# Optimization experiments

Hardware: AMD Instinct MI355X
Metric: run time of the kernel (lower is better)

## Reference

```python
import jax, jax.numpy as jnp
import numpy as np
from jax import lax

# Mamba2 config (matches init_kwargs + mamba_ssm defaults)
B_SZ, SEQ = 8, 2048
D_MODEL, D_STATE, EXPAND, HEADDIM = 1024, 128, 2, 64
D_INNER = EXPAND * D_MODEL            # 2048
NHEADS = D_INNER // HEADDIM           # 32
NGROUPS, D_CONV, CHUNK = 1, 4, 128
CONV_DIM = D_INNER + 2 * NGROUPS * D_STATE
D_IN_PROJ = 2 * D_INNER + 2 * NGROUPS * D_STATE + NHEADS
VAR_NUM, EPS = 3, 1e-5


def setup_inputs() -> dict:
    key = jax.random.key(0)
    ks = jax.random.split(key, 10)
    return {
        "embed_data": jax.random.normal(ks[0], (B_SZ, SEQ, D_MODEL), jnp.float32),
        "in_proj_w": jax.random.normal(ks[1], (D_IN_PROJ, D_MODEL), jnp.float32) * 0.02,
        "conv_w": jax.random.normal(ks[2], (CONV_DIM, D_CONV), jnp.float32) * 0.2,
        "conv_b": jnp.zeros((CONV_DIM,), jnp.float32),
        "dt_bias": jnp.log(jnp.expm1(jax.random.uniform(ks[3], (NHEADS,), jnp.float32, 1e-3, 0.1))),
        "A_log": jnp.log(jax.random.uniform(ks[4], (NHEADS,), jnp.float32, 1.0, 16.0)),
        "D": jnp.ones((NHEADS,), jnp.float32),
        "norm_w": jnp.ones((D_INNER,), jnp.float32),
        "out_proj_w": jax.random.normal(ks[5], (D_MODEL, D_INNER), jnp.float32) * 0.02,
        "dec_w": jax.random.normal(ks[6], (VAR_NUM, D_MODEL), jnp.float32) * 0.02,
        "dec_b": jnp.zeros((VAR_NUM,), jnp.float32),
    }


def _segsum(a):
    # a: (b,h,c,L) -> (b,h,c,L,L) lower-triangular segment sums
    L = a.shape[-1]
    cs = jnp.cumsum(a, -1)
    ss = cs[..., :, None] - cs[..., None, :]
    mask = jnp.tril(jnp.ones((L, L), bool))
    return jnp.where(mask, ss, -jnp.inf)


def _ssd(x, dt, A, Bm, Cm):
    # x:(b,l,h,p) dt:(b,l,h) A:(h,) Bm,Cm:(b,l,n); chunked SSD scan (Mamba2)
    b, l, h, p = x.shape
    n = Bm.shape[-1]
    c = l // CHUNK
    xc = x.reshape(b, c, CHUNK, h, p)
    dtc = dt.reshape(b, c, CHUNK, h)
    Bc = Bm.reshape(b, c, CHUNK, n)
    Cc = Cm.reshape(b, c, CHUNK, n)
    ac = (dt * A).reshape(b, c, CHUNK, h).transpose(0, 3, 1, 2)  # (b,h,c,L)
    acs = jnp.cumsum(ac, -1)
    Lmat = jnp.exp(_segsum(ac))                                   # (b,h,c,L,L)
    xdt = xc * dtc[..., None]
    # intra-chunk (diagonal block) outputs
    CB = jnp.einsum('bcln,bcsn->bcls', Cc, Bc)
    Y_diag = jnp.einsum('bcls,bhcls,bcshp->bclhp', CB, Lmat, xdt)
    # per-chunk final states
    decay_states = jnp.exp(acs[..., -1:] - acs)                   # (b,h,c,L)
    states = jnp.einsum('bcln,bhcl,bclhp->bchpn', Bc, decay_states, xdt)
    chunk_decay = jnp.exp(acs[..., -1])                           # (b,h,c)
    def step(carry, inp):
        st, dec = inp
        return carry * dec[..., None, None] + st, carry
    _, states_in = lax.scan(step, jnp.zeros((b, h, p, n), x.dtype),
                            (jnp.moveaxis(states, 1, 0), jnp.moveaxis(chunk_decay, 2, 0)))
    states_in = jnp.moveaxis(states_in, 0, 1)                     # (b,c,h,p,n)
    # inter-chunk (off-diagonal) contribution
    Y_off = jnp.einsum('bcln,bchpn,bhcl->bclhp', Cc, states_in, jnp.exp(acs))
    return (Y_diag + Y_off).reshape(b, l, h, p)


def reference(embed_data, in_proj_w, conv_w, conv_b, dt_bias, A_log, D, norm_w, out_proj_w, dec_w, dec_b):
    b, l, _ = embed_data.shape
    zxbcdt = embed_data @ in_proj_w.T                             # (b,l,D_IN_PROJ)
    z = zxbcdt[..., :D_INNER]
    xBC = zxbcdt[..., D_INNER:D_INNER + CONV_DIM]
    dt = jax.nn.softplus(zxbcdt[..., D_INNER + CONV_DIM:] + dt_bias)  # (b,l,h)
    # causal depthwise conv1d + SiLU
    xt = lax.conv_general_dilated(xBC.transpose(0, 2, 1), conv_w[:, None, :], (1,),
                                  [(D_CONV - 1, 0)], feature_group_count=CONV_DIM,
                                  dimension_numbers=('NCH', 'OIH', 'NCH'))
    xBC = jax.nn.silu(xt.transpose(0, 2, 1) + conv_b)
    x = xBC[..., :D_INNER].reshape(b, l, NHEADS, HEADDIM)
    Bm = xBC[..., D_INNER:D_INNER + D_STATE]
    Cm = xBC[..., D_INNER + D_STATE:]
    A = -jnp.exp(A_log)
    y = _ssd(x, dt, A, Bm, Cm) + D[None, None, :, None] * x
    # gated RMSNorm
    y = y.reshape(b, l, D_INNER) * jax.nn.silu(z)
    y = y * lax.rsqrt(jnp.mean(y * y, -1, keepdims=True) + EPS) * norm_w
    hidden = y @ out_proj_w.T
    pred = hidden @ dec_w.T + dec_b
    return pred, hidden
```

## Files before the change

### kernel.cpp

```cpp
#include <hip/hip_runtime.h>
#include <cstdint>

#define DEVI __device__ __forceinline__

typedef unsigned short u16;
typedef unsigned int u32;
typedef __attribute__((ext_vector_type(4))) float f32x4;
typedef __attribute__((ext_vector_type(8))) u16 u16x8;
typedef __attribute__((ext_vector_type(4))) u16 u16x4;
typedef __attribute__((ext_vector_type(8))) __bf16 bf16x8;

#define SEQL 2048
#define NBATCH 8
#define MROWS (NBATCH*SEQL)
#define DMODEL 1024
#define DINNER 2048
#define NHEADS 32
#define HEADD 64
#define DSTATE 128
#define CONVD 2304
#define NPROJ 4384
#define NPROJP 4608
#define CHUNKL 128
#define NCHUNK 16
#define PADC 136

DEVI float bf2f(u16 v){ u32 u = ((u32)v)<<16; return __builtin_bit_cast(float,u); }
DEVI u16 f2bf(float f){ u32 u = __builtin_bit_cast(u32,f); u32 r = (u + 0x7fffu + ((u>>16)&1u))>>16; return (u16)r; }

DEVI void gld_lds16(const void* g, void* lds){
  __builtin_amdgcn_global_load_lds(
    (const __attribute__((address_space(1))) void*)(uintptr_t)g,
    (__attribute__((address_space(3))) void*)(u32)(uintptr_t)lds, 16, 0, 0);
}

DEVI f32x4 MFMA(u16x8 a, u16x8 b, f32x4 c){
  return __builtin_amdgcn_mfma_f32_16x16x32_bf16(
      __builtin_bit_cast(bf16x8,a), __builtin_bit_cast(bf16x8,b), c, 0,0,0);
}

__global__ void k_sentinel(float* o){ o[0] = 12345.0f; }

__global__ __launch_bounds__(256) void k_cvt3(const float* __restrict__ e, u16* __restrict__ eb,
    const float* __restrict__ w1, u16* __restrict__ w1b,
    const float* __restrict__ w2, u16* __restrict__ w2b)
{
  int bid = blockIdx.x;
  const float* src; u16* dst; long n; long base;
  if (bid < 16384){ src = e;  dst = eb;  n = (long)MROWS*DMODEL;  base = (long)bid*1024; }
  else if (bid < 20992){ src = w1; dst = w1b; n = (long)NPROJ*DMODEL; base = (long)(bid-16384)*1024; }
  else { src = w2; dst = w2b; n = (long)DMODEL*DINNER; base = (long)(bid-20992)*1024; }
  long idx = base + (long)threadIdx.x*4;
  u16x4 o;
  if (idx < n){
    f32x4 v = *(const f32x4*)(src+idx);
    o[0]=f2bf(v[0]); o[1]=f2bf(v[1]); o[2]=f2bf(v[2]); o[3]=f2bf(v[3]);
  } else { o[0]=0; o[1]=0; o[2]=0; o[3]=0; }
  *(u16x4*)(dst+idx) = o;
}

#define STG(mat, h, ts) do { \
    const int d_ = (ts) & 1; \
    const size_t ko_ = (size_t)(((ts) < NT) ? (ts) : (NT-1)) * 64; \
    gld_lds16(sbase[mat][h][0] + ko_, (char*)lds + (mat)*65536 + (d_*2+(h))*16384 + tid*16); \
    gld_lds16(sbase[mat][h][1] + ko_, (char*)lds + (mat)*65536 + (d_*2+(h))*16384 + 8192 + tid*16); \
  } while(0)

#define LDA8(AF, d_, qm) { \
    _Pragma("unroll") for (int mf=0; mf<4; mf++) \
    _Pragma("unroll") for (int ks=0; ks<2; ks++) \
      AF[mf][ks] = *(const u16x8*)(lds + (size_t)((d_)*2+wm)*8192 + ((qm)*64+mf*16+lidx)*64 + ((ks*4+krow)^(lidx&7))*8); }

#define LDB4(BF, d_, qn) { \
    _Pragma("unroll") for (int nf=0; nf<2; nf++) \
    _Pragma("unroll") for (int ks=0; ks<2; ks++) \
      BF[nf][ks] = *(const u16x8*)(lds + 32768 + (size_t)((d_)*2+(wn>>1))*8192 + ((wn&1)*64+(qn)*32+nf*16+lidx)*64 + ((ks*4+krow)^(lidx&7))*8); }

#define MMAQ(QM, QN, AF, BF) { \
    _Pragma("unroll") for (int mf=0; mf<4; mf++) \
    _Pragma("unroll") for (int nf=0; nf<2; nf++) \
    _Pragma("unroll") for (int ks=0; ks<2; ks++) \
      acc[(QM)*4+mf][(QN)*2+nf] = MFMA(AF[mf][ks], BF[nf][ks], acc[(QM)*4+mf][(QN)*2+nf]); }

#define LHINT asm volatile("s_waitcnt lgkmcnt(8)" ::: "memory");

#define BAR1 __builtin_amdgcn_sched_barrier(0); __builtin_amdgcn_s_barrier(); \
    asm volatile("s_waitcnt lgkmcnt(0)" ::: "memory"); __builtin_amdgcn_sched_barrier(0); \
    __builtin_amdgcn_s_setprio(1);
#define BAR2 __builtin_amdgcn_s_setprio(0); __builtin_amdgcn_sched_barrier(0); \
    __builtin_amdgcn_s_barrier(); __builtin_amdgcn_sched_barrier(0);

template<int MODE>
__global__ __launch_bounds__(512, 2) void k_gemm8(const u16* __restrict__ A, const u16* __restrict__ Bt,
    const int K, const int Ndim, float* __restrict__ outF,
    u16* __restrict__ z_out, u16* __restrict__ xbc_out, float* __restrict__ dtraw_out)
{
  extern __shared__ u16 lds[];
  const int NT = K >> 6;
  const int tid = threadIdx.x;
  const int lane = tid & 63, wid = tid >> 6;
  const int wm = wid >> 2, wn = wid & 3;
  const int lidx = lane & 15, krow = lane >> 4;
  const int nmt = gridDim.x, nnt = gridDim.y;
  const int nwg = nmt * nnt;
  const int orig = blockIdx.y * nmt + blockIdx.x;
  const int qq = nwg >> 3, rr = nwg & 7;
  const int xcd = orig & 7, li = orig >> 3;
  const int pid = (xcd < rr ? xcd*(qq+1) : rr*(qq+1) + (xcd-rr)*qq) + li;
  const int GM = 8;
  const int npg = GM * nnt;
  const int gid = pid / npg;
  const int rem = pid % npg;
  const int m0 = (gid*GM + (rem & (GM-1))) * 256;
  const int n0 = (rem / GM) * 256;

  f32x4 acc[8][4];
  const f32x4 zf = {0.f,0.f,0.f,0.f};
  #pragma unroll
  for (int i=0;i<8;i++)
    #pragma unroll
    for (int j=0;j<4;j++) acc[i][j] = zf;

  const int r0 = tid >> 3;
  const int gsw = ((tid & 7) ^ (r0 & 7)) * 8;
  const u16* sbase[2][2][2];
  #pragma unroll
  for (int h=0; h<2; h++)
    #pragma unroll
    for (int L=0; L<2; L++){
      sbase[0][h][L] = A  + (size_t)(m0 + h*128 + L*64 + r0)*K + gsw;
      sbase[1][h][L] = Bt + (size_t)(n0 + h*128 + L*64 + r0)*K + gsw;
    }

  STG(0,0,0); STG(0,1,0); STG(1,0,0); STG(1,1,0);
  asm volatile("s_waitcnt vmcnt(4)" ::: "memory");
  STG(0,0,1); STG(0,1,1); STG(1,0,1);
  asm volatile("s_waitcnt vmcnt(6)" ::: "memory");
  __builtin_amdgcn_sched_barrier(0);
  __builtin_amdgcn_s_barrier();
  __builtin_amdgcn_sched_barrier(0);

  u16x8 af[4][2], bf0[2][2], bf1[2][2];
  for (int t = 0; t < NT; t += 2){
    LDA8(af, 0, 0); LDB4(bf0, 0, 0); STG(1,1,t+1); LHINT;
    BAR1; MMAQ(0,0,af,bf0); BAR2;
    LDB4(bf1, 0, 1);
    BAR1; MMAQ(0,1,af,bf1); BAR2;
    LDA8(af, 0, 1); STG(1,0,t+2);
    BAR1; MMAQ(1,1,af,bf1); BAR2;
    STG(0,0,t+2); STG(0,1,t+2);
    asm volatile("s_waitcnt vmcnt(6)" ::: "memory");
    BAR1; MMAQ(1,0,af,bf0); BAR2;
    LDA8(af, 1, 0); LDB4(bf0, 1, 0); STG(1,1,t+2); LHINT;
    BAR1; MMAQ(0,0,af,bf0); BAR2;
    LDB4(bf1, 1, 1);
    BAR1; MMAQ(0,1,af,bf1); BAR2;
    LDA8(af, 1, 1); STG(1,0,t+3);
    BAR1; MMAQ(1,1,af,bf1); BAR2;
    STG(0,0,t+3); STG(0,1,t+3);
    asm volatile("s_waitcnt vmcnt(6)" ::: "memory");
    BAR1; MMAQ(1,0,af,bf0); BAR2;
  }
  asm volatile("s_waitcnt vmcnt(0)" ::: "memory");

  #pragma unroll
  for (int im=0; im<8; im++)
    #pragma unroll
    for (int in=0; in<4; in++)
      #pragma unroll
      for (int r=0; r<4; r++){
        int gm = m0 + wm*128 + im*16 + krow*4 + r;
        int gn = n0 + wn*64 + in*16 + lidx;
        float v = acc[im][in][r];
        if (MODE==0){
          outF[(long)gm*Ndim + gn] = v;
        } else {
          if (gn < DINNER) z_out[(long)gm*DINNER + gn] = f2bf(v);
          else if (gn < DINNER+CONVD) xbc_out[(long)gm*CONVD + (gn-DINNER)] = f2bf(v);
          else if (gn < NPROJ) dtraw_out[(long)gm*NHEADS + (gn-DINNER-CONVD)] = v;
        }
      }
}

__global__ __launch_bounds__(128) void k_dtprep(const float* __restrict__ dtraw, const float* __restrict__ dt_bias,
    const float* __restrict__ A_log, float* __restrict__ dt_t, float* __restrict__ acs_t)
{
  int b = blockIdx.x >> 9;
  int h = (blockIdx.x >> 4) & 31;
  int c = blockIdx.x & 15;
  int l = threadIdx.x;
  int gl = c*128 + l;
  float raw = dtraw[((long)(b*SEQL + gl))*NHEADS + h] + dt_bias[h];
  float dt = (raw > 20.f) ? raw : log1pf(expf(raw));
  float A = -expf(A_log[h]);
  float ac = dt*A;
  __shared__ float ss[128];
  ss[l] = ac; __syncthreads();
  for (int o=1;o<128;o<<=1){
    float v = (l>=o)? ss[l-o] : 0.f;
    __syncthreads();
    ss[l] += v;
    __syncthreads();
  }
  float acs = ss[l];
  dt_t[((long)(b*NHEADS+h))*SEQL + gl] = dt;
  acs_t[((long)(b*NHEADS+h))*SEQL + gl] = acs;
}

__global__ __launch_bounds__(256) void k_conv(const u16* __restrict__ xbc, const float* __restrict__ conv_w,
    const float* __restrict__ conv_b, const float* __restrict__ dt_t,
    u16* __restrict__ xdtT, u16* __restrict__ BTt, u16* __restrict__ CTt)
{
  __shared__ u16 sm[131*64];
  int idx = blockIdx.x;
  int b = idx / 576; int rem = idx % 576; int cbk = rem >> 4; int lb = rem & 15;
  int ch0 = cbk*64, l0 = lb*128;
  for (int g = threadIdx.x; g < 131*8; g += 256){
    int r = g >> 3, cg = g & 7;
    int gl = l0 - 3 + r;
    u16x8 v;
    if (gl >= 0) v = *(const u16x8*)(xbc + ((long)(b*SEQL+gl))*CONVD + ch0 + cg*8);
    else { v[0]=0;v[1]=0;v[2]=0;v[3]=0;v[4]=0;v[5]=0;v[6]=0;v[7]=0; }
    *(u16x8*)(&sm[r*64 + cg*8]) = v;
  }
  __syncthreads();
  int ci = threadIdx.x & 63, g4 = threadIdx.x >> 6;
  int chg = ch0 + ci;
  f32x4 wv = *(const f32x4*)(conv_w + chg*4);
  float bia = conv_b[chg];
  bool isX = chg < DINNER;
  int h = chg >> 6; if (h > 31) h = 31;
  int p = chg & 63;
  const float* dtrow = dt_t + ((long)(b*NHEADS+h))*SEQL + l0 + g4*32;
  u16x8 ov[4];
  #pragma unroll
  for (int i=0;i<32;i++){
    int lr = g4*32 + i;
    float a = bia + wv[0]*bf2f(sm[(lr+0)*64+ci]) + wv[1]*bf2f(sm[(lr+1)*64+ci])
                  + wv[2]*bf2f(sm[(lr+2)*64+ci]) + wv[3]*bf2f(sm[(lr+3)*64+ci]);
    float s = a / (1.f + __expf(-a));
    if (isX) s *= dtrow[i];
    ov[i>>3][i&7] = f2bf(s);
  }
  u16* dst;
  if (isX)                      dst = xdtT + (((long)(b*NHEADS+h))*HEADD + p)*SEQL + l0 + g4*32;
  else if (chg < DINNER+DSTATE) dst = BTt + ((long)(b*DSTATE + (chg-DINNER)))*SEQL + l0 + g4*32;
  else                          dst = CTt + ((long)(b*DSTATE + (chg-DINNER-DSTATE)))*SEQL + l0 + g4*32;
  #pragma unroll
  for (int q=0;q<4;q++) *(u16x8*)(dst + q*8) = ov[q];
}

__global__ __launch_bounds__(256) void k_cbpar(const u16* __restrict__ BTt, const u16* __restrict__ CTt,
    const u16* __restrict__ xdtT, const float* __restrict__ acs_t,
    u16* __restrict__ CBm, u16* __restrict__ Cn, u16* __restrict__ states)
{
  __shared__ __align__(16) char smem[69632];
  const int tid = threadIdx.x;
  const int lane = tid & 63, wid = tid >> 6;
  const int lidx = lane & 15, krow = lane >> 4;
  const f32x4 zf = {0.f,0.f,0.f,0.f};
  if (blockIdx.x < 128){
    u16* Cl = (u16*)smem;
    u16* Bl = (u16*)(smem + 34816);
    int b = blockIdx.x >> 4, c = blockIdx.x & 15;
    for (int g = tid; g < 2048; g += 256){
      int n = g >> 4, lg = g & 15;
      u16x8 vc = *(const u16x8*)(CTt + ((long)(b*DSTATE+n))*SEQL + c*CHUNKL + lg*8);
      u16x8 vb = *(const u16x8*)(BTt + ((long)(b*DSTATE+n))*SEQL + c*CHUNKL + lg*8);
      #pragma unroll
      for (int j=0;j<8;j++){
        Cl[(lg*8+j)*136 + n] = vc[j];
        Bl[(lg*8+j)*136 + n] = vb[j];
      }
    }
    __syncthreads();
    const int wr = wid & 1, wc2 = wid >> 1;
    f32x4 acc[4][4];
    #pragma unroll
    for (int i=0;i<4;i++)
      #pragma unroll
      for (int j=0;j<4;j++) acc[i][j] = zf;
    #pragma unroll
    for (int k0=0;k0<128;k0+=32){
      u16x8 af[4], bfv[4];
      #pragma unroll
      for (int i=0;i<4;i++){
        af[i]  = *(const u16x8*)(&Cl[(wr*64+i*16+lidx)*136 + k0 + krow*8]);
        bfv[i] = *(const u16x8*)(&Bl[(wc2*64+i*16+lidx)*136 + k0 + krow*8]);
      }
      #pragma unroll
      for (int i=0;i<4;i++)
        #pragma unroll
        for (int j=0;j<4;j++)
          acc[i][j] = MFMA(af[i], bfv[j], acc[i][j]);
    }
    long base = ((long)(b*16+c))*128*128;
    #pragma unroll
    for (int i=0;i<4;i++)
      #pragma unroll
      for (int j=0;j<4;j++)
        #pragma unroll
        for (int r=0;r<4;r++){
          int l = wr*64+i*16+krow*4+r;
          int s = wc2*64+j*16+lidx;
          CBm[base + (long)l*128 + s] = f2bf(acc[i][j][r]);
        }
    for (int g = tid; g < 2048; g += 256){
      int l = g >> 4, ng = g & 15;
      u16x8 o;
      #pragma unroll
      for (int j=0;j<8;j++) o[j] = Cl[l*136 + ng*8 + j];
      *(u16x8*)(Cn + ((long)(b*SEQL + c*CHUNKL + l))*DSTATE + ng*8) = o;
    }
  } else {
    u16* Bs = (u16*)smem;
    u16* Xs = (u16*)(smem + 34816);
    float* acs_s = (float*)(smem + 52224);
    float* dec_s = (float*)(smem + 52736);
    const int idx = blockIdx.x - 128;
    const int c = idx & 15, bh = idx >> 4, b = bh >> 5;
    const int wps = wid & 1, wns = wid >> 1;
    const float* acs_g = acs_t + (long)bh*SEQL + c*128;
    const u16* X_g = xdtT + (long)bh*HEADD*SEQL + c*128;
    const u16* B_g = BTt + (long)b*DSTATE*SEQL + c*128;
    if (tid < 128) acs_s[tid] = acs_g[tid];
    __syncthreads();
    if (tid < 128) dec_s[tid] = __expf(acs_s[127] - acs_s[tid]);
    __syncthreads();
    for (int g = tid; g < 2048; g += 256){
      int n = g >> 4, lg = g & 15;
      u16x8 v = *(const u16x8*)(B_g + (long)n*SEQL + lg*8);
      u16x8 o;
      #pragma unroll
      for (int j=0;j<8;j++) o[j] = f2bf(bf2f(v[j])*dec_s[lg*8+j]);
      *(u16x8*)(&Bs[n*PADC + lg*8]) = o;
    }
    for (int g = tid; g < 1024; g += 256){
      int p = g >> 4, lg = g & 15;
      *(u16x8*)(&Xs[p*PADC + lg*8]) = *(const u16x8*)(X_g + (long)p*SEQL + lg*8);
    }
    __syncthreads();
    f32x4 accS[2][4];
    #pragma unroll
    for (int i=0;i<2;i++){ accS[i][0]=zf; accS[i][1]=zf; accS[i][2]=zf; accS[i][3]=zf; }
    #pragma unroll
    for (int k0=0;k0<128;k0+=32){
      u16x8 as2[2], bs2[4];
      #pragma unroll
      for (int i=0;i<2;i++) as2[i] = *(const u16x8*)(&Xs[(wps*32+i*16+lidx)*PADC + k0 + krow*8]);
      #pragma unroll
      for (int j=0;j<4;j++) bs2[j] = *(const u16x8*)(&Bs[(wns*64+j*16+lidx)*PADC + k0 + krow*8]);
      #pragma unroll
      for (int i=0;i<2;i++)
        #pragma unroll
        for (int j=0;j<4;j++)
          accS[i][j] = MFMA(as2[i], bs2[j], accS[i][j]);
    }
    u16* Sg = states + (long)idx*8192;
    #pragma unroll
    for (int i=0;i<2;i++)
      #pragma unroll
      for (int j=0;j<4;j++)
        #pragma unroll
        for (int r=0;r<4;r++){
          int p = wps*32 + i*16 + krow*4 + r;
          int n = wns*64 + j*16 + lidx;
          Sg[p*128 + n] = f2bf(accS[i][j][r]);
        }
  }
}

__global__ __launch_bounds__(256) void k_scan(u16* __restrict__ states, const float* __restrict__ acs_t)
{
  long gid = (long)blockIdx.x*256 + threadIdx.x;
  int bh = (int)(gid >> 11);
  int q = (int)(gid & 2047);
  __shared__ float cds[16];
  if (threadIdx.x < 16) cds[threadIdx.x] = __expf(acs_t[(long)bh*SEQL + threadIdx.x*128 + 127]);
  __syncthreads();
  u16* p = states + (long)bh*NCHUNK*8192 + q*4;
  u16x4 sv[16];
  #pragma unroll
  for (int c=0;c<16;c++) sv[c] = *(const u16x4*)(p + c*8192);
  float c0=0.f,c1=0.f,c2=0.f,c3=0.f;
  #pragma unroll
  for (int c=0;c<16;c++){
    u16x4 o; o[0]=f2bf(c0); o[1]=f2bf(c1); o[2]=f2bf(c2); o[3]=f2bf(c3);
    *(u16x4*)(p + c*8192) = o;
    float cd = cds[c];
    c0 = c0*cd + bf2f(sv[c][0]);
    c1 = c1*cd + bf2f(sv[c][1]);
    c2 = c2*cd + bf2f(sv[c][2]);
    c3 = c3*cd + bf2f(sv[c][3]);
  }
}

__global__ __launch_bounds__(256) void k_yoff(
    const u16* __restrict__ Cng, const u16* __restrict__ xdtT, const u16* __restrict__ CBm,
    const u16* __restrict__ SI, const float* __restrict__ acs_t, const float* __restrict__ dt_t,
    const float* __restrict__ Dparam, u16* __restrict__ y)
{
  __shared__ u16 Ts[128*PADC];
  __shared__ u16 Us[64*PADC];
  __shared__ float acs_s[128], dtr_s[128], eacs_s[128];
  const int idx = blockIdx.x;
  const int c = idx & 15, bh = idx >> 4, b = bh >> 5, h = bh & 31;
  const int tid = threadIdx.x, lane = tid & 63, wid = tid >> 6;
  const int lidx = lane & 15, krow = lane >> 4;
  const int wl = wid & 1, wp = wid >> 1;
  const float Dh = Dparam[h];
  const float* acs_g = acs_t + (long)bh*SEQL + c*128;
  const float* dt_g  = dt_t  + (long)bh*SEQL + c*128;
  const u16* X_g = xdtT + (long)bh*HEADD*SEQL + c*128;
  const u16* C_g = Cng + ((long)(b*SEQL + c*128))*DSTATE;
  const u16* CB_g = CBm + ((long)(b*NCHUNK + c))*CHUNKL*CHUNKL;
  const u16* SI_g = SI + (long)idx*8192;
  if (tid < 128){ acs_s[tid] = acs_g[tid]; dtr_s[tid] = dt_g[tid]; }
  __syncthreads();
  if (tid < 128) eacs_s[tid] = __expf(acs_s[tid]);
  __syncthreads();
  {
    int l = tid >> 1, s0 = (tid & 1)*64;
    float al = acs_s[l];
    #pragma unroll
    for (int qq=0;qq<8;qq++){
      u16x8 v = *(const u16x8*)(CB_g + (long)l*CHUNKL + s0 + qq*8);
      u16x8 o;
      #pragma unroll
      for (int j=0;j<8;j++){
        int s = s0 + qq*8 + j;
        float pv = (s <= l) ? bf2f(v[j]) * __expf(al - acs_s[s]) : 0.f;
        o[j] = f2bf(pv);
      }
      *(u16x8*)(&Ts[l*PADC + s0 + qq*8]) = o;
    }
  }
  for (int g = tid; g < 1024; g += 256){
    int p = g >> 4, lg = g & 15;
    *(u16x8*)(&Us[p*PADC + lg*8]) = *(const u16x8*)(X_g + (long)p*SEQL + lg*8);
  }
  __syncthreads();
  const f32x4 zf = {0.f,0.f,0.f,0.f};
  f32x4 accY[4][2];
  #pragma unroll
  for (int i=0;i<4;i++){ accY[i][0]=zf; accY[i][1]=zf; }
  #pragma unroll
  for (int k0=0;k0<128;k0+=32){
    u16x8 af[4], bfv[2];
    #pragma unroll
    for (int i=0;i<4;i++) af[i] = *(const u16x8*)(&Ts[(wl*64+i*16+lidx)*PADC + k0 + krow*8]);
    #pragma unroll
    for (int j=0;j<2;j++) bfv[j] = *(const u16x8*)(&Us[(wp*32+j*16+lidx)*PADC + k0 + krow*8]);
    #pragma unroll
    for (int i=0;i<4;i++)
      #pragma unroll
      for (int j=0;j<2;j++)
        accY[i][j] = MFMA(af[i], bfv[j], accY[i][j]);
  }
  #pragma unroll
  for (int i=0;i<4;i++)
    #pragma unroll
    for (int j=0;j<2;j++)
      #pragma unroll
      for (int r=0;r<4;r++){
        int l = wl*64 + i*16 + krow*4 + r;
        int p = wp*32 + j*16 + lidx;
        accY[i][j][r] += Dh * bf2f(Us[p*PADC + l]) / dtr_s[l];
      }
  __syncthreads();
  for (int g = tid; g < 2048; g += 256){
    int l = g >> 4, cb = g & 15;
    u16x8 v = *(const u16x8*)(C_g + (long)l*DSTATE + cb*8);
    float e = eacs_s[l];
    u16x8 o;
    #pragma unroll
    for (int j=0;j<8;j++) o[j] = f2bf(bf2f(v[j])*e);
    *(u16x8*)(&Ts[l*PADC + cb*8]) = o;
  }
  for (int g = tid; g < 1024; g += 256){
    int p = g >> 4, lg = g & 15;
    *(u16x8*)(&Us[p*PADC + lg*8]) = *(const u16x8*)(SI_g + p*128 + lg*8);
  }
  __syncthreads();
  #pragma unroll
  for (int k0=0;k0<128;k0+=32){
    u16x8 af[4], bfv[2];
    #pragma unroll
    for (int i=0;i<4;i++) af[i] = *(const u16x8*)(&Ts[(wl*64+i*16+lidx)*PADC + k0 + krow*8]);
    #pragma unroll
    for (int j=0;j<2;j++) bfv[j] = *(const u16x8*)(&Us[(wp*32+j*16+lidx)*PADC + k0 + krow*8]);
    #pragma unroll
    for (int i=0;i<4;i++)
      #pragma unroll
      for (int j=0;j<2;j++)
        accY[i][j] = MFMA(af[i], bfv[j], accY[i][j]);
  }
  #pragma unroll
  for (int i=0;i<4;i++)
    #pragma unroll
    for (int j=0;j<2;j++)
      #pragma unroll
      for (int r=0;r<4;r++){
        int l = wl*64 + i*16 + krow*4 + r;
        int p = wp*32 + j*16 + lidx;
        y[((long)(b*SEQL + c*128 + l))*DINNER + h*HEADD + p] = f2bf(accY[i][j][r]);
      }
}

__global__ __launch_bounds__(256) void k_ssd(
    const u16* __restrict__ Cng, const u16* __restrict__ BTt, const u16* __restrict__ xdtT,
    const u16* __restrict__ CBm, const float* __restrict__ acs_t, const float* __restrict__ dt_t,
    const float* __restrict__ Dparam, u16* __restrict__ y)
{
  __shared__ u16 Cs[128*PADC];
  __shared__ u16 Bs[128*PADC];
  __shared__ u16 Ps[128*PADC];
  __shared__ u16 Xs[64*PADC];
  __shared__ float carry[64*132];
  __shared__ float acs_s[128], eacs_s[128], dec_s[128], dtr_s[128];
  const int bh = blockIdx.x;
  const int b = bh >> 5, h = bh & 31;
  const int tid = threadIdx.x, lane = tid & 63, wid = tid >> 6;
  const int lidx = lane & 15, krow = lane >> 4;
  const int wl = wid & 1, wp = wid >> 1;
  const int wps = wid & 1, wns = wid >> 1;
  for (int i = tid; i < 64*132; i += 256) carry[i] = 0.f;
  const float Dh = Dparam[h];
  const float* acs_g = acs_t + (long)bh*SEQL;
  const float* dt_g = dt_t + (long)bh*SEQL;
  const u16* X_g = xdtT + (long)bh*HEADD*SEQL;
  const u16* B_g = BTt + (long)b*DSTATE*SEQL;
  const u16* C_g = Cng + (long)b*SEQL*DSTATE;
  const u16* CB_g = CBm + (long)b*NCHUNK*CHUNKL*CHUNKL;
  const f32x4 zf = {0.f,0.f,0.f,0.f};
  for (int c=0;c<NCHUNK;c++){
    __syncthreads();
    if (tid < 128){ acs_s[tid] = acs_g[c*128+tid]; dtr_s[tid] = dt_g[c*128+tid]; }
    __syncthreads();
    if (tid < 128){ float a = acs_s[tid]; eacs_s[tid] = __expf(a); dec_s[tid] = __expf(acs_s[127]-a); }
    __syncthreads();
    for (int g = tid; g < 2048; g += 256){
      int l = g >> 4, cb = g & 15;
      u16x8 v = *(const u16x8*)(C_g + ((long)(c*128+l))*DSTATE + cb*8);
      float e = eacs_s[l];
      u16x8 o;
      #pragma unroll
      for (int j=0;j<8;j++) o[j] = f2bf(bf2f(v[j])*e);
      *(u16x8*)(&Cs[l*PADC + cb*8]) = o;
    }
    for (int g = tid; g < 2048; g += 256){
      int n = g >> 4, lg = g & 15;
      u16x8 v = *(const u16x8*)(B_g + (long)n*SEQL + c*128 + lg*8);
      u16x8 o;
      #pragma unroll
      for (int j=0;j<8;j++) o[j] = f2bf(bf2f(v[j])*dec_s[lg*8+j]);
      *(u16x8*)(&Bs[n*PADC + lg*8]) = o;
    }
    for (int g = tid; g < 1024; g += 256){
      int p = g >> 4, lg = g & 15;
      *(u16x8*)(&Xs[p*PADC + lg*8]) = *(const u16x8*)(X_g + (long)p*SEQL + c*128 + lg*8);
    }
    {
      int l = tid >> 1, s0 = (tid & 1)*64;
      float al = acs_s[l];
      #pragma unroll
      for (int q=0;q<8;q++){
        u16x8 v = *(const u16x8*)(CB_g + ((long)(c*128+l))*CHUNKL + s0 + q*8);
        u16x8 o;
        #pragma unroll
        for (int j=0;j<8;j++){
          int s = s0 + q*8 + j;
          float pv = (s <= l) ? bf2f(v[j]) * __expf(al - acs_s[s]) : 0.f;
          o[j] = f2bf(pv);
        }
        *(u16x8*)(&Ps[l*PADC + s0 + q*8]) = o;
      }
    }
    __syncthreads();
    f32x4 accY[4][2];
    f32x4 accS[2][4];
    #pragma unroll
    for (int i=0;i<4;i++){ accY[i][0]=zf; accY[i][1]=zf; }
    #pragma unroll
    for (int i=0;i<2;i++){ accS[i][0]=zf; accS[i][1]=zf; accS[i][2]=zf; accS[i][3]=zf; }
    #pragma unroll
    for (int k0=0;k0<128;k0+=32){
      u16x8 af[4], bfv[2];
      #pragma unroll
      for (int i=0;i<4;i++) af[i] = *(const u16x8*)(&Cs[(wl*64+i*16+lidx)*PADC + k0 + krow*8]);
      #pragma unroll
      for (int j=0;j<2;j++){
        const float* cp = &carry[(wp*32+j*16+lidx)*132 + k0 + krow*8];
        f32x4 c0 = *(const f32x4*)cp;
        f32x4 c1 = *(const f32x4*)(cp+4);
        u16x8 o;
        o[0]=f2bf(c0[0]); o[1]=f2bf(c0[1]); o[2]=f2bf(c0[2]); o[3]=f2bf(c0[3]);
        o[4]=f2bf(c1[0]); o[5]=f2bf(c1[1]); o[6]=f2bf(c1[2]); o[7]=f2bf(c1[3]);
        bfv[j] = o;
      }
      #pragma unroll
      for (int i=0;i<4;i++)
        #pragma unroll
        for (int j=0;j<2;j++)
          accY[i][j] = MFMA(af[i], bfv[j], accY[i][j]);
    }
    #pragma unroll
    for (int k0=0;k0<128;k0+=32){
      u16x8 af[4], bfv[2];
      #pragma unroll
      for (int i=0;i<4;i++) af[i] = *(const u16x8*)(&Ps[(wl*64+i*16+lidx)*PADC + k0 + krow*8]);
      #pragma unroll
      for (int j=0;j<2;j++) bfv[j] = *(const u16x8*)(&Xs[(wp*32+j*16+lidx)*PADC + k0 + krow*8]);
      #pragma unroll
      for (int i=0;i<4;i++)
        #pragma unroll
        for (int j=0;j<2;j++)
          accY[i][j] = MFMA(af[i], bfv[j], accY[i][j]);
    }
    #pragma unroll
    for (int k0=0;k0<128;k0+=32){
      u16x8 as2[2], bs2[4];
      #pragma unroll
      for (int i=0;i<2;i++) as2[i] = *(const u16x8*)(&Xs[(wps*32+i*16+lidx)*PADC + k0 + krow*8]);
      #pragma unroll
      for (int j=0;j<4;j++) bs2[j] = *(const u16x8*)(&Bs[(wns*64+j*16+lidx)*PADC + k0 + krow*8]);
      #pragma unroll
      for (int i=0;i<2;i++)
        #pragma unroll
        for (int j=0;j<4;j++)
          accS[i][j] = MFMA(as2[i], bs2[j], accS[i][j]);
    }
    __syncthreads();
    float cd = __expf(acs_s[127]);
    #pragma unroll
    for (int i=0;i<2;i++)
      #pragma unroll
      for (int j=0;j<4;j++)
        #pragma unroll
        for (int r=0;r<4;r++){
          int p = wps*32 + i*16 + krow*4 + r;
          int n = wns*64 + j*16 + lidx;
          carry[p*132+n] = carry[p*132+n]*cd + accS[i][j][r];
        }
    #pragma unroll
    for (int i=0;i<4;i++)
      #pragma unroll
      for (int j=0;j<2;j++)
        #pragma unroll
        for (int r=0;r<4;r++){
          int l = wl*64 + i*16 + krow*4 + r;
          int p = wp*32 + j*16 + lidx;
          float xv = bf2f(Xs[p*PADC + l]) / dtr_s[l];
          float val = accY[i][j][r] + Dh*xv;
          y[((long)(b*SEQL + c*128 + l))*DINNER + h*HEADD + p] = f2bf(val);
        }
  }
}

__global__ __launch_bounds__(256) void k_gate(const u16* __restrict__ y, const u16* __restrict__ z,
    const float* __restrict__ norm_w, u16* __restrict__ out)
{
  long row = blockIdx.x;
  const u16* yr = y + row*DINNER;
  const u16* zr = z + row*DINNER;
  int t = threadIdx.x;
  u16x8 yy = *(const u16x8*)(yr + t*8);
  u16x8 zz = *(const u16x8*)(zr + t*8);
  float g[8]; float ss = 0.f;
  #pragma unroll
  for (int j=0;j<8;j++){
    float zfv = bf2f(zz[j]);
    float sg = zfv / (1.f + __expf(-zfv));
    float gv = bf2f(yy[j]) * sg;
    g[j] = gv; ss += gv*gv;
  }
  #pragma unroll
  for (int o=32;o>0;o>>=1) ss += __shfl_down(ss, o);
  __shared__ float part[4];
  int lane = t & 63, wid = t>>6;
  if (lane==0) part[wid] = ss;
  __syncthreads();
  float tot = part[0]+part[1]+part[2]+part[3];
  float inv = rsqrtf(tot*(1.f/DINNER) + 1e-5f);
  u16x8 o;
  #pragma unroll
  for (int j=0;j<8;j++) o[j] = f2bf(g[j]*inv*norm_w[t*8+j]);
  *(u16x8*)(out + row*DINNER + t*8) = o;
}

__global__ __launch_bounds__(256) void k_pred(const float* __restrict__ hid, const float* __restrict__ dec_w,
    const float* __restrict__ dec_b, float* __restrict__ pred)
{
  int t = threadIdx.x;
  long row = (long)blockIdx.x*8 + (t>>5);
  int lk = t & 31;
  const float* hr = hid + row*DMODEL;
  float a0=0.f,a1=0.f,a2=0.f;
  #pragma unroll
  for (int i=0;i<8;i++){
    f32x4 hv = *(const f32x4*)(hr + lk*4 + i*128);
    f32x4 w0 = *(const f32x4*)(dec_w + 0*DMODEL + lk*4 + i*128);
    f32x4 w1 = *(const f32x4*)(dec_w + 1*DMODEL + lk*4 + i*128);
    f32x4 w2 = *(const f32x4*)(dec_w + 2*DMODEL + lk*4 + i*128);
    a0 += hv[0]*w0[0]+hv[1]*w0[1]+hv[2]*w0[2]+hv[3]*w0[3];
    a1 += hv[0]*w1[0]+hv[1]*w1[1]+hv[2]*w1[2]+hv[3]*w1[3];
    a2 += hv[0]*w2[0]+hv[1]*w2[1]+hv[2]*w2[2]+hv[3]*w2[3];
  }
  #pragma unroll
  for (int o=16;o>0;o>>=1){
    a0 += __shfl_down(a0,o,32); a1 += __shfl_down(a1,o,32); a2 += __shfl_down(a2,o,32);
  }
  if (lk==0){
    pred[row*3+0] = a0 + dec_b[0];
    pred[row*3+1] = a1 + dec_b[1];
    pred[row*3+2] = a2 + dec_b[2];
  }
}

extern "C" void kernel_launch(void* const* d_in, const int* in_sizes, int n_in,
                              void* d_out, int out_size, void* d_ws, size_t ws_size,
                              hipStream_t stream)
{
  const float* embed      = (const float*)d_in[0];
  const float* in_proj_w  = (const float*)d_in[1];
  const float* conv_w     = (const float*)d_in[2];
  const float* conv_b     = (const float*)d_in[3];
  const float* dt_bias    = (const float*)d_in[4];
  const float* A_log      = (const float*)d_in[5];
  const float* Dp         = (const float*)d_in[6];
  const float* norm_w     = (const float*)d_in[7];
  const float* out_proj_w = (const float*)d_in[8];
  const float* dec_w      = (const float*)d_in[9];
  const float* dec_b      = (const float*)d_in[10];

  char* ws = (char*)d_ws;
  size_t off = 0;
  auto alloc = [&](size_t bytes)->void*{ void* p = ws + off; off += (bytes + 255) & ~(size_t)255; return p; };

  u16* xbc = (u16*)alloc((size_t)MROWS*CONVD*2);
  u16* yb  = xbc;
  u16* R2  = (u16*)alloc((size_t)MROWS*DINNER*2);
  u16* Ebf = R2;
  u16* W1  = R2 + (size_t)MROWS*DMODEL;
  u16* xdtT  = R2;
  u16* ynorm = R2;
  float* dtraw = (float*)alloc((size_t)MROWS*NHEADS*4);
  float* dt_t  = (float*)alloc((size_t)NBATCH*NHEADS*SEQL*4);
  float* acs   = (float*)alloc((size_t)NBATCH*NHEADS*SEQL*4);
  u16* BTt   = (u16*)alloc((size_t)NBATCH*DSTATE*SEQL*2);
  u16* CTt   = (u16*)alloc((size_t)NBATCH*DSTATE*SEQL*2);
  u16* Cn    = (u16*)alloc((size_t)NBATCH*SEQL*DSTATE*2);
  u16* CBm   = (u16*)alloc((size_t)NBATCH*NCHUNK*CHUNKL*CHUNKL*2);
  u16* W2    = (u16*)alloc((size_t)DMODEL*DINNER*2);

  size_t off_base = off;
  u16* S = (u16*)alloc((size_t)NBATCH*NHEADS*NCHUNK*HEADD*DSTATE*2);
  bool use_par = (off <= ws_size);

  if (off_base > ws_size){
    k_sentinel<<<1,1,0,stream>>>((float*)d_out);
    return;
  }

  float* pred   = (float*)d_out;
  float* hidden = (float*)d_out + (size_t)MROWS*3;
  u16* zb = (u16*)hidden;

  hipFuncSetAttribute((const void*)k_gemm8<1>, hipFuncAttributeMaxDynamicSharedMemorySize, 131072);
  hipFuncSetAttribute((const void*)k_gemm8<0>, hipFuncAttributeMaxDynamicSharedMemorySize, 131072);

  k_cvt3<<<23040,256,0,stream>>>(embed, Ebf, in_proj_w, W1, out_proj_w, W2);
  {
    dim3 g1(64, NPROJP/256);
    k_gemm8<1><<<g1,512,131072,stream>>>(Ebf, W1, DMODEL, 0, nullptr, zb, xbc, dtraw);
  }
  k_dtprep<<<4096,128,0,stream>>>(dtraw, dt_bias, A_log, dt_t, acs);
  k_conv<<<4608,256,0,stream>>>(xbc, conv_w, conv_b, dt_t, xdtT, BTt, CTt);
  k_cbpar<<<(use_par ? 4224 : 128),256,0,stream>>>(BTt, CTt, xdtT, acs, CBm, Cn, S);
  if (use_par){
    k_scan<<<2048,256,0,stream>>>(S, acs);
    k_yoff<<<4096,256,0,stream>>>(Cn, xdtT, CBm, S, acs, dt_t, Dp, yb);
  } else {
    k_ssd<<<256,256,0,stream>>>(Cn, BTt, xdtT, CBm, acs, dt_t, Dp, yb);
  }
  k_gate<<<16384,256,0,stream>>>(yb, zb, norm_w, ynorm);
  {
    dim3 g2(64, DMODEL/256);
    k_gemm8<0><<<g2,512,131072,stream>>>(ynorm, W2, DINNER, DMODEL, hidden, nullptr, nullptr, nullptr);
  }
  k_pred<<<2048,256,0,stream>>>(hidden, dec_w, dec_b, pred);
}
```

Baseline: 532.1 us.

## Drop LDS wait hint in GEMM, slide conv window, batch gate rows per block

Three unrelated tweaks. The GEMM main loop loses its partial lgkmcnt wait hint before the first barrier. The depthwise conv keeps a sliding window of four converted values in registers, so each step does one LDS load and conversion instead of four. The gate/RMSNorm kernel handles four rows per block with norm weights hoisted, cutting the grid by 4x at the cost of an extra barrier per row and less parallelism.

```diff
diff --git a/kernel.cpp b/kernel.cpp
--- a/kernel.cpp
+++ b/kernel.cpp
@@ -81,8 +81,6 @@
     _Pragma("unroll") for (int nf=0; nf<2; nf++) \
     _Pragma("unroll") for (int ks=0; ks<2; ks++) \
       acc[(QM)*4+mf][(QN)*2+nf] = MFMA(AF[mf][ks], BF[nf][ks], acc[(QM)*4+mf][(QN)*2+nf]); }
-
-#define LHINT asm volatile("s_waitcnt lgkmcnt(8)" ::: "memory");
 
 #define BAR1 __builtin_amdgcn_sched_barrier(0); __builtin_amdgcn_s_barrier(); \
     asm volatile("s_waitcnt lgkmcnt(0)" ::: "memory"); __builtin_amdgcn_sched_barrier(0); \
@@ -142,7 +140,7 @@
 
   u16x8 af[4][2], bf0[2][2], bf1[2][2];
   for (int t = 0; t < NT; t += 2){
-    LDA8(af, 0, 0); LDB4(bf0, 0, 0); STG(1,1,t+1); LHINT;
+    LDA8(af, 0, 0); LDB4(bf0, 0, 0); STG(1,1,t+1);
     BAR1; MMAQ(0,0,af,bf0); BAR2;
     LDB4(bf1, 0, 1);
     BAR1; MMAQ(0,1,af,bf1); BAR2;
@@ -151,7 +149,7 @@
     STG(0,0,t+2); STG(0,1,t+2);
     asm volatile("s_waitcnt vmcnt(6)" ::: "memory");
     BAR1; MMAQ(1,0,af,bf0); BAR2;
-    LDA8(af, 1, 0); LDB4(bf0, 1, 0); STG(1,1,t+2); LHINT;
+    LDA8(af, 1, 0); LDB4(bf0, 1, 0); STG(1,1,t+2);
     BAR1; MMAQ(0,0,af,bf0); BAR2;
     LDB4(bf1, 1, 1);
     BAR1; MMAQ(0,1,af,bf1); BAR2;
@@ -233,11 +231,15 @@
   int p = chg & 63;
   const float* dtrow = dt_t + ((long)(b*NHEADS+h))*SEQL + l0 + g4*32;
   u16x8 ov[4];
+  const int baseR = g4*32;
+  float w0, w1 = bf2f(sm[(baseR+0)*64+ci]);
+  float w2 = bf2f(sm[(baseR+1)*64+ci]);
+  float w3 = bf2f(sm[(baseR+2)*64+ci]);
   #pragma unroll
   for (int i=0;i<32;i++){
-    int lr = g4*32 + i;
-    float a = bia + wv[0]*bf2f(sm[(lr+0)*64+ci]) + wv[1]*bf2f(sm[(lr+1)*64+ci])
-                  + wv[2]*bf2f(sm[(lr+2)*64+ci]) + wv[3]*bf2f(sm[(lr+3)*64+ci]);
+    w0 = w1; w1 = w2; w2 = w3;
+    w3 = bf2f(sm[(baseR+i+3)*64+ci]);
+    float a = bia + wv[0]*w0 + wv[1]*w1 + wv[2]*w2 + wv[3]*w3;
     float s = a / (1.f + __expf(-a));
     if (isX) s *= dtrow[i];
     ov[i>>3][i&7] = f2bf(s);
@@ -660,32 +662,37 @@
 __global__ __launch_bounds__(256) void k_gate(const u16* __restrict__ y, const u16* __restrict__ z,
     const float* __restrict__ norm_w, u16* __restrict__ out)
 {
-  long row = blockIdx.x;
-  const u16* yr = y + row*DINNER;
-  const u16* zr = z + row*DINNER;
   int t = threadIdx.x;
-  u16x8 yy = *(const u16x8*)(yr + t*8);
-  u16x8 zz = *(const u16x8*)(zr + t*8);
-  float g[8]; float ss = 0.f;
-  #pragma unroll
-  for (int j=0;j<8;j++){
-    float zfv = bf2f(zz[j]);
-    float sg = zfv / (1.f + __expf(-zfv));
-    float gv = bf2f(yy[j]) * sg;
-    g[j] = gv; ss += gv*gv;
-  }
-  #pragma unroll
-  for (int o=32;o>0;o>>=1) ss += __shfl_down(ss, o);
+  int lane = t & 63, wid = t>>6;
   __shared__ float part[4];
-  int lane = t & 63, wid = t>>6;
-  if (lane==0) part[wid] = ss;
-  __syncthreads();
-  float tot = part[0]+part[1]+part[2]+part[3];
-  float inv = rsqrtf(tot*(1.f/DINNER) + 1e-5f);
-  u16x8 o;
-  #pragma unroll
-  for (int j=0;j<8;j++) o[j] = f2bf(g[j]*inv*norm_w[t*8+j]);
-  *(u16x8*)(out + row*DINNER + t*8) = o;
+  float nw[8];
+  #pragma unroll
+  for (int j=0;j<8;j++) nw[j] = norm_w[t*8+j];
+  #pragma unroll
+  for (int rr=0; rr<4; rr++){
+    long row = (long)blockIdx.x*4 + rr;
+    u16x8 yy = *(const u16x8*)(y + row*DINNER + t*8);
+    u16x8 zz = *(const u16x8*)(z + row*DINNER + t*8);
+    float g[8]; float ss = 0.f;
+    #pragma unroll
+    for (int j=0;j<8;j++){
+      float zfv = bf2f(zz[j]);
+      float sg = zfv / (1.f + __expf(-zfv));
+      float gv = bf2f(yy[j]) * sg;
+      g[j] = gv; ss += gv*gv;
+    }
+    #pragma unroll
+    for (int o=32;o>0;o>>=1) ss += __shfl_down(ss, o);
+    if (lane==0) part[wid] = ss;
+    __syncthreads();
+    float tot = part[0]+part[1]+part[2]+part[3];
+    float inv = rsqrtf(tot*(1.f/DINNER) + 1e-5f);
+    u16x8 o;
+    #pragma unroll
+    for (int j=0;j<8;j++) o[j] = f2bf(g[j]*inv*nw[j]);
+    *(u16x8*)(out + row*DINNER + t*8) = o;
+    __syncthreads();
+  }
 }
 
 __global__ __launch_bounds__(256) void k_pred(const float* __restrict__ hid, const float* __restrict__ dec_w,
@@ -783,7 +790,7 @@
   } else {
     k_ssd<<<256,256,0,stream>>>(Cn, BTt, xdtT, CBm, acs, dt_t, Dp, yb);
   }
-  k_gate<<<16384,256,0,stream>>>(yb, zb, norm_w, ynorm);
+  k_gate<<<4096,256,0,stream>>>(yb, zb, norm_w, ynorm);
   {
     dim3 g2(64, DMODEL/256);
     k_gemm8<0><<<g2,512,131072,stream>>>(ynorm, W2, DINNER, DMODEL, hidden, nullptr, nullptr, nullptr);
```

Result: no change. 537.8 us (+1.1%).
